# Kernel tuning notes

Measured on AMD Instinct MI355X. Metric: run time of the kernel, lower is better.

The kernel has to match this reference:

```python
import jax, jax.numpy as jnp
import numpy as np

BATCH, INPUT_SIZE, STEPS = 256, 512, 256
HIDDEN = 512


def setup_inputs() -> dict:
    key = jax.random.key(0)
    ks = jax.random.split(key, 5)
    s = 1.0 / np.sqrt(HIDDEN)
    return {
        "x": jax.random.normal(ks[0], (BATCH, INPUT_SIZE, STEPS), dtype=jnp.float32),
        "weight_ih": jax.random.uniform(ks[1], (3 * HIDDEN, INPUT_SIZE), jnp.float32, -s, s),
        "weight_hh": jax.random.uniform(ks[2], (3 * HIDDEN, HIDDEN), jnp.float32, -s, s),
        "bias_ih": jax.random.uniform(ks[3], (3 * HIDDEN,), jnp.float32, -s, s),
        "bias_hh": jax.random.uniform(ks[4], (3 * HIDDEN,), jnp.float32, -s, s),
    }


def reference(x, weight_ih, weight_hh, bias_ih, bias_hh):
    # x: [B, input_size, steps]; run a GRUCell over the time axis, return final hidden.
    B = x.shape[0]
    # Precompute all input projections in one big GEMM: [steps, B, 3H]
    gi_all = jnp.einsum('bis,gi->sbg', x, weight_ih) + bias_ih

    def step(h, gi):
        gh = h @ weight_hh.T + bias_hh  # [B, 3H]
        i_r, i_z, i_n = jnp.split(gi, 3, axis=-1)
        h_r, h_z, h_n = jnp.split(gh, 3, axis=-1)
        r = jax.nn.sigmoid(i_r + h_r)
        z = jax.nn.sigmoid(i_z + h_z)
        n = jnp.tanh(i_n + r * h_n)
        h_new = (1.0 - z) * n + z * h
        return h_new, None

    h0 = jnp.zeros((B, HIDDEN), dtype=x.dtype)
    h_final, _ = jax.lax.scan(step, h0, gi_all)
    return h_final
```

## Files before the change

### kernel.cpp

```cpp
#include <hip/hip_runtime.h>
#include <stdint.h>

typedef __attribute__((ext_vector_type(8))) short bf16x8;
typedef __attribute__((ext_vector_type(4))) short s16x4;
typedef __attribute__((ext_vector_type(4))) float f32x4;
typedef __attribute__((ext_vector_type(4))) unsigned u32x4;

#define AS1 __attribute__((address_space(1)))
#define AS3 __attribute__((address_space(3)))

static __device__ __forceinline__ void gload_lds16(const void* g, void* l) {
  __builtin_amdgcn_global_load_lds((const AS1 unsigned int*)g,
                                   (AS3 unsigned int*)l, 16, 0, 0);
}

static __device__ __forceinline__ short f2bs(float f) {
  unsigned u = __builtin_bit_cast(unsigned, f);
  unsigned r = (u + 0x7fffu + ((u >> 16) & 1u)) >> 16;
  return (short)r;
}
static __device__ __forceinline__ float bs2f(short s) {
  unsigned u = ((unsigned)(unsigned short)s) << 16;
  return __builtin_bit_cast(float, u);
}

static __device__ __forceinline__ float sigmoid_f(float x) {
  return 1.0f / (1.0f + __expf(-x));
}
static __device__ __forceinline__ float tanh_f(float x) {
  float ax = fabsf(x);
  float e  = __expf(-2.0f * ax);
  float t  = (1.0f - e) / (1.0f + e);
  return copysignf(t, x);
}

#define BATCH 256
#define HID   512
#define STEPS 256
#define G3    1536

__global__ __launch_bounds__(256) void convert_kernel(const float* __restrict__ src,
                                                      short* __restrict__ dst, int n4) {
  int i = blockIdx.x * 256 + threadIdx.x;
  if (i < n4) {
    float4 v = *(const float4*)(src + (size_t)i * 4);
    s16x4 o;
    o[0] = f2bs(v.x); o[1] = f2bs(v.y); o[2] = f2bs(v.z); o[3] = f2bs(v.w);
    *(s16x4*)(dst + (size_t)i * 4) = o;
  }
}

__global__ __launch_bounds__(256) void transpose_kernel(const float* __restrict__ x,
                                                        short* __restrict__ xT) {
  int bx = blockIdx.x;
  int st = bx & 7, it = (bx >> 3) & 15, b = bx >> 7;
  int s0 = st * 32, i0 = it * 32;
  int tid = threadIdx.x;
  __shared__ float tile[32][33];
  int il = tid >> 3, s4 = (tid & 7) * 4;
  float4 v = *(const float4*)(x + (size_t)b * 131072 + (size_t)(i0 + il) * 256 + s0 + s4);
  tile[il][s4 + 0] = v.x; tile[il][s4 + 1] = v.y;
  tile[il][s4 + 2] = v.z; tile[il][s4 + 3] = v.w;
  __syncthreads();
  int sl = tid >> 3, iv = (tid & 7) * 4;
  s16x4 o;
  o[0] = f2bs(tile[iv + 0][sl]); o[1] = f2bs(tile[iv + 1][sl]);
  o[2] = f2bs(tile[iv + 2][sl]); o[3] = f2bs(tile[iv + 3][sl]);
  *(s16x4*)(xT + (size_t)(s0 + sl) * 131072 + (size_t)b * 512 + i0 + iv) = o;
}

__global__ __launch_bounds__(256) void phase1_kernel(const short* __restrict__ A,
                                                     const short* __restrict__ B,
                                                     const float* __restrict__ bias,
                                                     short* __restrict__ out, int M) {
  int MT = M >> 7;
  int bx = blockIdx.x;
  int mt = bx % MT, nt = bx / MT;
  int m0 = mt * 128, n0 = nt * 128;
  int tid = threadIdx.x, w = tid >> 6, lane = tid & 63;
  int lm = lane & 15, q = lane >> 4;
  int wm = w & 1, wn = w >> 1;
  __shared__ short As[128 * 32];
  __shared__ short Bs[128 * 32];
  f32x4 acc[4][4] = {};
  int srow = lane >> 2;
  int scol = (lane & 3) * 8;

  for (int kt = 0; kt < 16; ++kt) {
#pragma unroll
    for (int i2 = 0; i2 < 2; ++i2) {
      int i = w * 2 + i2;
      int row = i * 16 + srow;
      gload_lds16(A + (size_t)(m0 + row) * 512 + kt * 32 + scol, As + i * 512);
      gload_lds16(B + (size_t)(n0 + row) * 512 + kt * 32 + scol, Bs + i * 512);
    }
    __syncthreads();
    bf16x8 av[4], bv[4];
#pragma unroll
    for (int f = 0; f < 4; ++f) {
      av[f] = *(const bf16x8*)(As + (wm * 64 + f * 16 + lm) * 32 + q * 8);
      bv[f] = *(const bf16x8*)(Bs + (wn * 64 + f * 16 + lm) * 32 + q * 8);
    }
#pragma unroll
    for (int fm = 0; fm < 4; ++fm)
#pragma unroll
      for (int fn = 0; fn < 4; ++fn)
        acc[fm][fn] = __builtin_amdgcn_mfma_f32_16x16x32_bf16(av[fm], bv[fn], acc[fm][fn], 0, 0, 0);
    __syncthreads();
  }
#pragma unroll
  for (int fn = 0; fn < 4; ++fn) {
    int g = n0 + wn * 64 + fn * 16 + lm;
    float bi = bias[g];
#pragma unroll
    for (int fm = 0; fm < 4; ++fm) {
      int rb = m0 + wm * 64 + fm * 16 + q * 4;
#pragma unroll
      for (int r = 0; r < 4; ++r)
        out[(size_t)(rb + r) * G3 + g] = f2bs(acc[fm][fn][r] + bi);
    }
  }
}

__global__ __launch_bounds__(256) void scan_kernel(const short* __restrict__ gi,
                                                   const short* __restrict__ Whh,
                                                   const float* __restrict__ bias_hh,
                                                   unsigned* __restrict__ hbuf,
                                                   float* __restrict__ hmaster,
                                                   int CH, int step_base, int first) {
  int bid = blockIdx.x;
  int xcd = bid & 7, slot = bid >> 3;
  int group = xcd + 8 * (slot >> 4);
  int j = slot & 15;
  int tid = threadIdx.x;
  int w = tid >> 6, lane = tid & 63;
  int lm = lane & 15, q = lane >> 4;
  int grow = group * 16;

  __shared__ short h_lds[16 * 520];
  __shared__ float gh_lds[16][100];
  __shared__ float h_loc[512];
  __shared__ float bhh[96];

  bf16x8 Bf[2][16];
  if (w < 3) {
#pragma unroll
    for (int tau = 0; tau < 2; ++tau)
#pragma unroll
      for (int kt = 0; kt < 16; ++kt) {
        int row = w * 512 + j * 32 + tau * 16 + lm;
        Bf[tau][kt] = *(const bf16x8*)(Whh + (size_t)row * 512 + kt * 32 + q * 8);
      }
  }

  if (tid < 96) {
    int p = tid >> 5, cc = tid & 31;
    bhh[tid] = bias_hh[p * 512 + j * 32 + cc];
  }
#pragma unroll
  for (int u = 0; u < 2; ++u) {
    int idx = tid + u * 256;
    int r = idx >> 5, cc = idx & 31;
    h_loc[idx] = first ? 0.0f : hmaster[(size_t)(grow + r) * 512 + j * 32 + cc];
  }
  __syncthreads();

  int i0 = tid, i1 = tid + 256;
  const short* gp0 = gi + (size_t)(grow + (i0 >> 5)) * G3 + j * 32 + (i0 & 31);
  const short* gp1 = gi + (size_t)(grow + (i1 >> 5)) * G3 + j * 32 + (i1 & 31);
  const size_t gstride = (size_t)256 * G3;

  short pg0r = gp0[0], pg0z = gp0[512], pg0n = gp0[1024];
  short pg1r = gp1[0], pg1z = gp1[512], pg1n = gp1[1024];

  unsigned o0 = (unsigned)tid * 16u;
  const int r0 = tid >> 7;
  const int colb = (tid & 127) * 4;
  short* lp = h_lds + r0 * 520 + colb;
  unsigned* grp_base = hbuf + (size_t)group * 8192;

  for (int t = 0; t < CH; ++t) {
    int gstep = step_base + t;
    int p = gstep & 1;
    const unsigned* src = grp_base + (size_t)p * 131072;
    unsigned want = (unsigned)gstep;

    u32x4 v0, v1, v2, v3, v4, v5, v6, v7;
    int spin = 0;
    for (;;) {
      asm volatile(
          "global_load_dwordx4 %0, %8, %16 sc0 sc1\n\t"
          "global_load_dwordx4 %1, %9, %16 sc0 sc1\n\t"
          "global_load_dwordx4 %2, %10, %16 sc0 sc1\n\t"
          "global_load_dwordx4 %3, %11, %16 sc0 sc1\n\t"
          "global_load_dwordx4 %4, %12, %16 sc0 sc1\n\t"
          "global_load_dwordx4 %5, %13, %16 sc0 sc1\n\t"
          "global_load_dwordx4 %6, %14, %16 sc0 sc1\n\t"
          "global_load_dwordx4 %7, %15, %16 sc0 sc1\n\t"
          "s_waitcnt vmcnt(0)"
          : "=&v"(v0), "=&v"(v1), "=&v"(v2), "=&v"(v3),
            "=&v"(v4), "=&v"(v5), "=&v"(v6), "=&v"(v7)
          : "v"(o0), "v"(o0 + 4096u), "v"(o0 + 8192u), "v"(o0 + 12288u),
            "v"(o0 + 16384u), "v"(o0 + 20480u), "v"(o0 + 24576u), "v"(o0 + 28672u),
            "s"(src)
          : "memory");
      unsigned d;
      d  = (v0[0] ^ want) | (v0[1] ^ want) | (v0[2] ^ want) | (v0[3] ^ want);
      d |= (v1[0] ^ want) | (v1[1] ^ want) | (v1[2] ^ want) | (v1[3] ^ want);
      d |= (v2[0] ^ want) | (v2[1] ^ want) | (v2[2] ^ want) | (v2[3] ^ want);
      d |= (v3[0] ^ want) | (v3[1] ^ want) | (v3[2] ^ want) | (v3[3] ^ want);
      d |= (v4[0] ^ want) | (v4[1] ^ want) | (v4[2] ^ want) | (v4[3] ^ want);
      d |= (v5[0] ^ want) | (v5[1] ^ want) | (v5[2] ^ want) | (v5[3] ^ want);
      d |= (v6[0] ^ want) | (v6[1] ^ want) | (v6[2] ^ want) | (v6[3] ^ want);
      d |= (v7[0] ^ want) | (v7[1] ^ want) | (v7[2] ^ want) | (v7[3] ^ want);
      if (((d & 0xffffu) == 0u) || (++spin > (1 << 16))) break;
      __builtin_amdgcn_s_sleep(1);
    }

#define STASH(vv, c)                                                         \
    {                                                                        \
      s16x4 o_;                                                              \
      o_[0] = (short)(vv[0] >> 16); o_[1] = (short)(vv[1] >> 16);            \
      o_[2] = (short)(vv[2] >> 16); o_[3] = (short)(vv[3] >> 16);            \
      *(s16x4*)(lp + (c) * 1040) = o_;                                       \
    }
    STASH(v0, 0) STASH(v1, 1) STASH(v2, 2) STASH(v3, 3)
    STASH(v4, 4) STASH(v5, 5) STASH(v6, 6) STASH(v7, 7)
#undef STASH

    float cg0r = bs2f(pg0r), cg0z = bs2f(pg0z), cg0n = bs2f(pg0n);
    float cg1r = bs2f(pg1r), cg1z = bs2f(pg1z), cg1n = bs2f(pg1n);
    {
      size_t o = (size_t)((t + 1 < CH) ? (t + 1) : t) * gstride;
      pg0r = gp0[o]; pg0z = gp0[o + 512]; pg0n = gp0[o + 1024];
      pg1r = gp1[o]; pg1z = gp1[o + 512]; pg1n = gp1[o + 1024];
    }
    __syncthreads();

    if (w < 3) {
      f32x4 a0 = {0.f,0.f,0.f,0.f}, a1 = {0.f,0.f,0.f,0.f};
      f32x4 a2 = {0.f,0.f,0.f,0.f}, a3 = {0.f,0.f,0.f,0.f};
#pragma unroll
      for (int kt = 0; kt < 8; ++kt) {
        bf16x8 a = *(const bf16x8*)(h_lds + lm * 520 + kt * 32 + q * 8);
        a0 = __builtin_amdgcn_mfma_f32_16x16x32_bf16(a, Bf[0][kt], a0, 0, 0, 0);
        a1 = __builtin_amdgcn_mfma_f32_16x16x32_bf16(a, Bf[1][kt], a1, 0, 0, 0);
      }
#pragma unroll
      for (int kt = 8; kt < 16; ++kt) {
        bf16x8 a = *(const bf16x8*)(h_lds + lm * 520 + kt * 32 + q * 8);
        a2 = __builtin_amdgcn_mfma_f32_16x16x32_bf16(a, Bf[0][kt], a2, 0, 0, 0);
        a3 = __builtin_amdgcn_mfma_f32_16x16x32_bf16(a, Bf[1][kt], a3, 0, 0, 0);
      }
#pragma unroll
      for (int r = 0; r < 4; ++r) {
        gh_lds[q * 4 + r][w * 32 + lm]      = a0[r] + a2[r];
        gh_lds[q * 4 + r][w * 32 + 16 + lm] = a1[r] + a3[r];
      }
    }
    __syncthreads();

    unsigned tagp = (unsigned)(gstep + 1);
    unsigned* dstb = grp_base + (size_t)(1 - p) * 131072;
    {
      int r = i0 >> 5, cc = i0 & 31;
      float hr = gh_lds[r][cc]      + bhh[cc];
      float hz = gh_lds[r][32 + cc] + bhh[32 + cc];
      float hn = gh_lds[r][64 + cc] + bhh[64 + cc];
      float rr = sigmoid_f(cg0r + hr);
      float zz = sigmoid_f(cg0z + hz);
      float nn = tanh_f(cg0n + rr * hn);
      float hv = (1.0f - zz) * nn + zz * h_loc[i0];
      h_loc[i0] = hv;
      unsigned val = (((unsigned)(unsigned short)f2bs(hv)) << 16) | tagp;
      unsigned* dp = dstb + r * 512 + j * 32 + cc;
      asm volatile("global_store_dword %0, %1, off sc0 sc1" :: "v"(dp), "v"(val) : "memory");
    }
    {
      int r = i1 >> 5, cc = i1 & 31;
      float hr = gh_lds[r][cc]      + bhh[cc];
      float hz = gh_lds[r][32 + cc] + bhh[32 + cc];
      float hn = gh_lds[r][64 + cc] + bhh[64 + cc];
      float rr = sigmoid_f(cg1r + hr);
      float zz = sigmoid_f(cg1z + hz);
      float nn = tanh_f(cg1n + rr * hn);
      float hv = (1.0f - zz) * nn + zz * h_loc[i1];
      h_loc[i1] = hv;
      unsigned val = (((unsigned)(unsigned short)f2bs(hv)) << 16) | tagp;
      unsigned* dp = dstb + r * 512 + j * 32 + cc;
      asm volatile("global_store_dword %0, %1, off sc0 sc1" :: "v"(dp), "v"(val) : "memory");
    }
  }

#pragma unroll
  for (int u = 0; u < 2; ++u) {
    int idx = tid + u * 256;
    int r = idx >> 5, cc = idx & 31;
    hmaster[(size_t)(grow + r) * 512 + j * 32 + cc] = h_loc[idx];
  }
}

extern "C" void kernel_launch(void* const* d_in, const int* in_sizes, int n_in,
                              void* d_out, int out_size, void* d_ws, size_t ws_size,
                              hipStream_t stream) {
  const float* x   = (const float*)d_in[0];
  const float* Wih = (const float*)d_in[1];
  const float* Whh = (const float*)d_in[2];
  const float* bih = (const float*)d_in[3];
  const float* bhh = (const float*)d_in[4];
  float* out = (float*)d_out;
  char* ws = (char*)d_ws;

  const size_t XT_BYTES   = (size_t)256 * 256 * 512 * 2;
  const size_t W_BYTES    = (size_t)1536 * 512 * 2;
  const size_t HBUF_BYTES = (size_t)2 * 256 * 512 * 4;
  const size_t FIXED = XT_BYTES + 2 * W_BYTES + HBUF_BYTES + 4096;

  int CH = 256;
  while (CH > 4 && FIXED + (size_t)CH * 256 * G3 * 2 > ws_size) CH >>= 1;

  size_t off = 0;
  short* gi = (short*)(ws + off);          off += (size_t)CH * 256 * G3 * 2;
  short* xT = (short*)(ws + off);          off += XT_BYTES;
  short* WihB = (short*)(ws + off);        off += W_BYTES;
  short* WhhB = (short*)(ws + off);        off += W_BYTES;
  unsigned* hbuf = (unsigned*)(ws + off);

  hipMemsetAsync(hbuf, 0, HBUF_BYTES, stream);

  convert_kernel<<<768, 256, 0, stream>>>(Wih, WihB, 196608);
  convert_kernel<<<768, 256, 0, stream>>>(Whh, WhhB, 196608);
  transpose_kernel<<<32768, 256, 0, stream>>>(x, xT);

  int nch = 256 / CH;
  for (int c = 0; c < nch; ++c) {
    int M = CH * 256;
    phase1_kernel<<<(M / 128) * 12, 256, 0, stream>>>(
        xT + (size_t)c * CH * 256 * 512, WihB, bih, gi, M);
    scan_kernel<<<256, 256, 0, stream>>>(gi, WhhB, bhh, hbuf, out,
                                         CH, c * CH, c == 0 ? 1 : 0);
  }
}
```

Measured before the change: 888.6 us.

## Split recurrent GEMM over K across all four waves, feed MFMA directly from registers

Each of the four waves now holds a K-quarter of the W_hh slice for all six output tiles and builds MFMA A-operands straight from the polled hidden-state registers, skipping the LDS staging of h. Partial sums are written to a double-buffered LDS area and reduced in the gate epilogue, which removes one __syncthreads per step and puts the fourth, previously idle wave to work. The cost is an extra cross-wave reduction over LDS and a changed polling address pattern. The spin limit is also halved.

```diff
diff --git a/kernel.cpp b/kernel.cpp
--- a/kernel.cpp
+++ b/kernel.cpp
@@ -32,6 +32,11 @@
   float e  = __expf(-2.0f * ax);
   float t  = (1.0f - e) / (1.0f + e);
   return copysignf(t, x);
+}
+
+static __device__ __forceinline__ unsigned stale8(u32x4 a, u32x4 b, unsigned want) {
+  return ((a[0] ^ want) | (a[1] ^ want) | (a[2] ^ want) | (a[3] ^ want) |
+          (b[0] ^ want) | (b[1] ^ want) | (b[2] ^ want) | (b[3] ^ want)) & 0xffffu;
 }
 
 #define BATCH 256
@@ -129,34 +134,28 @@
                                                    float* __restrict__ hmaster,
                                                    int CH, int step_base, int first) {
   int bid = blockIdx.x;
-  int xcd = bid & 7, slot = bid >> 3;
-  int group = xcd + 8 * (slot >> 4);
-  int j = slot & 15;
+  int group = (bid & 7) + 8 * ((bid >> 3) >> 4);
+  int j = (bid >> 3) & 15;
   int tid = threadIdx.x;
   int w = tid >> 6, lane = tid & 63;
   int lm = lane & 15, q = lane >> 4;
   int grow = group * 16;
 
-  __shared__ short h_lds[16 * 520];
-  __shared__ float gh_lds[16][100];
+  __shared__ float part[12288];
   __shared__ float h_loc[512];
   __shared__ float bhh[96];
 
-  bf16x8 Bf[2][16];
-  if (w < 3) {
-#pragma unroll
-    for (int tau = 0; tau < 2; ++tau)
-#pragma unroll
-      for (int kt = 0; kt < 16; ++kt) {
-        int row = w * 512 + j * 32 + tau * 16 + lm;
-        Bf[tau][kt] = *(const bf16x8*)(Whh + (size_t)row * 512 + kt * 32 + q * 8);
-      }
-  }
-
-  if (tid < 96) {
-    int p = tid >> 5, cc = tid & 31;
-    bhh[tid] = bias_hh[p * 512 + j * 32 + cc];
-  }
+  bf16x8 Wf[6][4];
+#pragma unroll
+  for (int n = 0; n < 6; ++n) {
+    int g = n >> 1, ch = n & 1;
+#pragma unroll
+    for (int i = 0; i < 4; ++i) {
+      int k = w * 4 + i;
+      Wf[n][i] = *(const bf16x8*)(Whh + (size_t)(g * 512 + j * 32 + ch * 16 + lm) * 512 + k * 32 + q * 8);
+    }
+  }
+  if (tid < 96) bhh[tid] = bias_hh[(tid >> 5) * 512 + j * 32 + (tid & 31)];
 #pragma unroll
   for (int u = 0; u < 2; ++u) {
     int idx = tid + u * 256;
@@ -169,64 +168,61 @@
   const short* gp0 = gi + (size_t)(grow + (i0 >> 5)) * G3 + j * 32 + (i0 & 31);
   const short* gp1 = gi + (size_t)(grow + (i1 >> 5)) * G3 + j * 32 + (i1 & 31);
   const size_t gstride = (size_t)256 * G3;
-
   short pg0r = gp0[0], pg0z = gp0[512], pg0n = gp0[1024];
   short pg1r = gp1[0], pg1z = gp1[512], pg1n = gp1[1024];
 
-  unsigned o0 = (unsigned)tid * 16u;
-  const int r0 = tid >> 7;
-  const int colb = (tid & 127) * 4;
-  short* lp = h_lds + r0 * 520 + colb;
-  unsigned* grp_base = hbuf + (size_t)group * 8192;
+  unsigned* grp = hbuf + (size_t)group * 8192;
+  unsigned o0 = (unsigned)(lm * 2048 + w * 512 + q * 32);
+  unsigned o1 = o0 + 128, o2 = o0 + 256, o3 = o0 + 384;
 
   for (int t = 0; t < CH; ++t) {
     int gstep = step_base + t;
     int p = gstep & 1;
-    const unsigned* src = grp_base + (size_t)p * 131072;
-    unsigned want = (unsigned)gstep;
+    const unsigned* src = grp + (size_t)p * 131072;
+    unsigned want = (unsigned)gstep & 0xffffu;
 
     u32x4 v0, v1, v2, v3, v4, v5, v6, v7;
     int spin = 0;
     for (;;) {
       asm volatile(
-          "global_load_dwordx4 %0, %8, %16 sc0 sc1\n\t"
-          "global_load_dwordx4 %1, %9, %16 sc0 sc1\n\t"
-          "global_load_dwordx4 %2, %10, %16 sc0 sc1\n\t"
-          "global_load_dwordx4 %3, %11, %16 sc0 sc1\n\t"
-          "global_load_dwordx4 %4, %12, %16 sc0 sc1\n\t"
-          "global_load_dwordx4 %5, %13, %16 sc0 sc1\n\t"
-          "global_load_dwordx4 %6, %14, %16 sc0 sc1\n\t"
-          "global_load_dwordx4 %7, %15, %16 sc0 sc1\n\t"
+          "global_load_dwordx4 %0, %8, %12 sc0 sc1\n\t"
+          "global_load_dwordx4 %1, %8, %12 offset:16 sc0 sc1\n\t"
+          "global_load_dwordx4 %2, %9, %12 sc0 sc1\n\t"
+          "global_load_dwordx4 %3, %9, %12 offset:16 sc0 sc1\n\t"
+          "global_load_dwordx4 %4, %10, %12 sc0 sc1\n\t"
+          "global_load_dwordx4 %5, %10, %12 offset:16 sc0 sc1\n\t"
+          "global_load_dwordx4 %6, %11, %12 sc0 sc1\n\t"
+          "global_load_dwordx4 %7, %11, %12 offset:16 sc0 sc1\n\t"
           "s_waitcnt vmcnt(0)"
           : "=&v"(v0), "=&v"(v1), "=&v"(v2), "=&v"(v3),
             "=&v"(v4), "=&v"(v5), "=&v"(v6), "=&v"(v7)
-          : "v"(o0), "v"(o0 + 4096u), "v"(o0 + 8192u), "v"(o0 + 12288u),
-            "v"(o0 + 16384u), "v"(o0 + 20480u), "v"(o0 + 24576u), "v"(o0 + 28672u),
-            "s"(src)
+          : "v"(o0), "v"(o1), "v"(o2), "v"(o3), "s"(src)
           : "memory");
-      unsigned d;
-      d  = (v0[0] ^ want) | (v0[1] ^ want) | (v0[2] ^ want) | (v0[3] ^ want);
-      d |= (v1[0] ^ want) | (v1[1] ^ want) | (v1[2] ^ want) | (v1[3] ^ want);
-      d |= (v2[0] ^ want) | (v2[1] ^ want) | (v2[2] ^ want) | (v2[3] ^ want);
-      d |= (v3[0] ^ want) | (v3[1] ^ want) | (v3[2] ^ want) | (v3[3] ^ want);
-      d |= (v4[0] ^ want) | (v4[1] ^ want) | (v4[2] ^ want) | (v4[3] ^ want);
-      d |= (v5[0] ^ want) | (v5[1] ^ want) | (v5[2] ^ want) | (v5[3] ^ want);
-      d |= (v6[0] ^ want) | (v6[1] ^ want) | (v6[2] ^ want) | (v6[3] ^ want);
-      d |= (v7[0] ^ want) | (v7[1] ^ want) | (v7[2] ^ want) | (v7[3] ^ want);
-      if (((d & 0xffffu) == 0u) || (++spin > (1 << 16))) break;
+      unsigned d = stale8(v0, v1, want) | stale8(v2, v3, want) |
+                   stale8(v4, v5, want) | stale8(v6, v7, want);
+      if (d == 0u || ++spin > (1 << 15)) break;
       __builtin_amdgcn_s_sleep(1);
     }
 
-#define STASH(vv, c)                                                         \
-    {                                                                        \
-      s16x4 o_;                                                              \
-      o_[0] = (short)(vv[0] >> 16); o_[1] = (short)(vv[1] >> 16);            \
-      o_[2] = (short)(vv[2] >> 16); o_[3] = (short)(vv[3] >> 16);            \
-      *(s16x4*)(lp + (c) * 1040) = o_;                                       \
-    }
-    STASH(v0, 0) STASH(v1, 1) STASH(v2, 2) STASH(v3, 3)
-    STASH(v4, 4) STASH(v5, 5) STASH(v6, 6) STASH(v7, 7)
-#undef STASH
+    f32x4 acc[6] = {};
+
+#define SLICE(ii, VA, VB)                                                     \
+    {                                                                         \
+      bf16x8 a;                                                               \
+      a[0] = (short)(VA[0] >> 16); a[1] = (short)(VA[1] >> 16);               \
+      a[2] = (short)(VA[2] >> 16); a[3] = (short)(VA[3] >> 16);               \
+      a[4] = (short)(VB[0] >> 16); a[5] = (short)(VB[1] >> 16);               \
+      a[6] = (short)(VB[2] >> 16); a[7] = (short)(VB[3] >> 16);               \
+      _Pragma("unroll")                                                       \
+      for (int n = 0; n < 6; ++n)                                             \
+        acc[n] = __builtin_amdgcn_mfma_f32_16x16x32_bf16(a, Wf[n][ii], acc[n], 0, 0, 0); \
+    }
+
+    SLICE(0, v0, v1)
+    SLICE(1, v2, v3)
+    SLICE(2, v4, v5)
+    SLICE(3, v6, v7)
+#undef SLICE
 
     float cg0r = bs2f(pg0r), cg0z = bs2f(pg0z), cg0n = bs2f(pg0n);
     float cg1r = bs2f(pg1r), cg1z = bs2f(pg1z), cg1n = bs2f(pg1n);
@@ -235,61 +231,44 @@
       pg0r = gp0[o]; pg0z = gp0[o + 512]; pg0n = gp0[o + 1024];
       pg1r = gp1[o]; pg1z = gp1[o + 512]; pg1n = gp1[o + 1024];
     }
+
+    {
+      float* pw = part + p * 6144 + w * 1536 + lane * 4;
+#pragma unroll
+      for (int n = 0; n < 6; ++n)
+        *(f32x4*)(pw + n * 256) = acc[n];
+    }
     __syncthreads();
 
-    if (w < 3) {
-      f32x4 a0 = {0.f,0.f,0.f,0.f}, a1 = {0.f,0.f,0.f,0.f};
-      f32x4 a2 = {0.f,0.f,0.f,0.f}, a3 = {0.f,0.f,0.f,0.f};
-#pragma unroll
-      for (int kt = 0; kt < 8; ++kt) {
-        bf16x8 a = *(const bf16x8*)(h_lds + lm * 520 + kt * 32 + q * 8);
-        a0 = __builtin_amdgcn_mfma_f32_16x16x32_bf16(a, Bf[0][kt], a0, 0, 0, 0);
-        a1 = __builtin_amdgcn_mfma_f32_16x16x32_bf16(a, Bf[1][kt], a1, 0, 0, 0);
-      }
-#pragma unroll
-      for (int kt = 8; kt < 16; ++kt) {
-        bf16x8 a = *(const bf16x8*)(h_lds + lm * 520 + kt * 32 + q * 8);
-        a2 = __builtin_amdgcn_mfma_f32_16x16x32_bf16(a, Bf[0][kt], a2, 0, 0, 0);
-        a3 = __builtin_amdgcn_mfma_f32_16x16x32_bf16(a, Bf[1][kt], a3, 0, 0, 0);
-      }
-#pragma unroll
-      for (int r = 0; r < 4; ++r) {
-        gh_lds[q * 4 + r][w * 32 + lm]      = a0[r] + a2[r];
-        gh_lds[q * 4 + r][w * 32 + 16 + lm] = a1[r] + a3[r];
-      }
-    }
-    __syncthreads();
-
     unsigned tagp = (unsigned)(gstep + 1);
-    unsigned* dstb = grp_base + (size_t)(1 - p) * 131072;
-    {
-      int r = i0 >> 5, cc = i0 & 31;
-      float hr = gh_lds[r][cc]      + bhh[cc];
-      float hz = gh_lds[r][32 + cc] + bhh[32 + cc];
-      float hn = gh_lds[r][64 + cc] + bhh[64 + cc];
-      float rr = sigmoid_f(cg0r + hr);
-      float zz = sigmoid_f(cg0z + hz);
-      float nn = tanh_f(cg0n + rr * hn);
-      float hv = (1.0f - zz) * nn + zz * h_loc[i0];
-      h_loc[i0] = hv;
-      unsigned val = (((unsigned)(unsigned short)f2bs(hv)) << 16) | tagp;
-      unsigned* dp = dstb + r * 512 + j * 32 + cc;
-      asm volatile("global_store_dword %0, %1, off sc0 sc1" :: "v"(dp), "v"(val) : "memory");
-    }
-    {
-      int r = i1 >> 5, cc = i1 & 31;
-      float hr = gh_lds[r][cc]      + bhh[cc];
-      float hz = gh_lds[r][32 + cc] + bhh[32 + cc];
-      float hn = gh_lds[r][64 + cc] + bhh[64 + cc];
-      float rr = sigmoid_f(cg1r + hr);
-      float zz = sigmoid_f(cg1z + hz);
-      float nn = tanh_f(cg1n + rr * hn);
-      float hv = (1.0f - zz) * nn + zz * h_loc[i1];
-      h_loc[i1] = hv;
-      unsigned val = (((unsigned)(unsigned short)f2bs(hv)) << 16) | tagp;
-      unsigned* dp = dstb + r * 512 + j * 32 + cc;
-      asm volatile("global_store_dword %0, %1, off sc0 sc1" :: "v"(dp), "v"(val) : "memory");
-    }
+    unsigned* dstb = grp + (size_t)(1 - p) * 131072;
+
+#define CELL(EE, CGR, CGZ, CGN)                                               \
+    {                                                                         \
+      int row = (EE) >> 5, colh = (EE) & 31;                                  \
+      const float* pp = part + p * 6144 + ((row >> 2) * 16 + (colh & 15)) * 4 \
+                        + (row & 3);                                          \
+      int nr = colh >> 4;                                                     \
+      float sr = 0.f, sz = 0.f, sn = 0.f;                                     \
+      _Pragma("unroll")                                                       \
+      for (int ww = 0; ww < 4; ++ww) {                                        \
+        const float* qq = pp + ww * 1536;                                     \
+        sr += qq[nr * 256]; sz += qq[(2 + nr) * 256]; sn += qq[(4 + nr) * 256]; \
+      }                                                                       \
+      float hr = sr + bhh[colh], hz = sz + bhh[32 + colh], hn = sn + bhh[64 + colh]; \
+      float rr = sigmoid_f(CGR + hr);                                         \
+      float zz = sigmoid_f(CGZ + hz);                                         \
+      float nn = tanh_f(CGN + rr * hn);                                       \
+      float hv = (1.0f - zz) * nn + zz * h_loc[EE];                           \
+      h_loc[EE] = hv;                                                         \
+      unsigned val = (((unsigned)(unsigned short)f2bs(hv)) << 16) | tagp;     \
+      unsigned* dp = dstb + row * 512 + j * 32 + colh;                        \
+      asm volatile("global_store_dword %0, %1, off sc0 sc1" :: "v"(dp), "v"(val) : "memory"); \
+    }
+
+    CELL(i0, cg0r, cg0z, cg0n)
+    CELL(i1, cg1r, cg1z, cg1n)
+#undef CELL
   }
 
 #pragma unroll
```

Result: slower. 1.173 ms (+32.0%).

## Repartition GRU scan into fewer, wider blocks with all waves doing MFMA

Applied to the files above, without the earlier changes.

The recurrent scan kernel goes from 256 blocks of 256 threads, each owning 32 hidden columns with 3 MFMA waves, to 64 blocks of 512 threads. Each block owns 128 hidden columns for a 16-row batch group, and all 8 waves compute all three gates over the full K of 512. This cuts the number of blocks that poll and publish hidden state each step and gives each block a larger share of the work. The cost is more weight registers per wave (48 fragments), a longer serial K chain per wave, and fewer CUs in use, which may reduce parallelism per step. The poll loop also loads half as much data per thread and has a lower spin cap.

```diff
diff --git a/kernel.cpp b/kernel.cpp
--- a/kernel.cpp
+++ b/kernel.cpp
@@ -32,6 +32,11 @@
   float e  = __expf(-2.0f * ax);
   float t  = (1.0f - e) / (1.0f + e);
   return copysignf(t, x);
+}
+
+static __device__ __forceinline__ unsigned stale8(u32x4 a, u32x4 b, unsigned want) {
+  return ((a[0] ^ want) | (a[1] ^ want) | (a[2] ^ want) | (a[3] ^ want) |
+          (b[0] ^ want) | (b[1] ^ want) | (b[2] ^ want) | (b[3] ^ want)) & 0xffffu;
 }
 
 #define BATCH 256
@@ -122,98 +127,78 @@
   }
 }
 
-__global__ __launch_bounds__(256) void scan_kernel(const short* __restrict__ gi,
-                                                   const short* __restrict__ Whh,
-                                                   const float* __restrict__ bias_hh,
-                                                   unsigned* __restrict__ hbuf,
-                                                   float* __restrict__ hmaster,
-                                                   int CH, int step_base, int first) {
+__global__ __launch_bounds__(512, 2) void scan_kernel(const short* __restrict__ gi,
+                                                      const short* __restrict__ Whh,
+                                                      const float* __restrict__ bias_hh,
+                                                      unsigned* __restrict__ hbuf,
+                                                      float* __restrict__ hmaster,
+                                                      int CH, int step_base, int first) {
   int bid = blockIdx.x;
   int xcd = bid & 7, slot = bid >> 3;
-  int group = xcd + 8 * (slot >> 4);
-  int j = slot & 15;
+  int j = slot & 3;
+  int group = xcd + 8 * (slot >> 2);
   int tid = threadIdx.x;
   int w = tid >> 6, lane = tid & 63;
   int lm = lane & 15, q = lane >> 4;
   int grow = group * 16;
 
   __shared__ short h_lds[16 * 520];
-  __shared__ float gh_lds[16][100];
-  __shared__ float h_loc[512];
-  __shared__ float bhh[96];
-
-  bf16x8 Bf[2][16];
-  if (w < 3) {
-#pragma unroll
-    for (int tau = 0; tau < 2; ++tau)
-#pragma unroll
-      for (int kt = 0; kt < 16; ++kt) {
-        int row = w * 512 + j * 32 + tau * 16 + lm;
-        Bf[tau][kt] = *(const bf16x8*)(Whh + (size_t)row * 512 + kt * 32 + q * 8);
-      }
-  }
-
-  if (tid < 96) {
-    int p = tid >> 5, cc = tid & 31;
-    bhh[tid] = bias_hh[p * 512 + j * 32 + cc];
-  }
-#pragma unroll
-  for (int u = 0; u < 2; ++u) {
-    int idx = tid + u * 256;
-    int r = idx >> 5, cc = idx & 31;
-    h_loc[idx] = first ? 0.0f : hmaster[(size_t)(grow + r) * 512 + j * 32 + cc];
+  __shared__ float gh_lds[16][388];
+  __shared__ float h_loc[2048];
+  __shared__ float bhh[384];
+
+  bf16x8 Wf[3][16];
+#pragma unroll
+  for (int g = 0; g < 3; ++g)
+#pragma unroll
+    for (int kt = 0; kt < 16; ++kt)
+      Wf[g][kt] = *(const bf16x8*)(Whh + (size_t)(g * 512 + j * 128 + w * 16 + lm) * 512 + kt * 32 + q * 8);
+
+  if (tid < 384) bhh[tid] = bias_hh[(tid >> 7) * 512 + j * 128 + (tid & 127)];
+#pragma unroll
+  for (int u = 0; u < 4; ++u) {
+    int idx = tid + u * 512;
+    int r = idx >> 7, cc = idx & 127;
+    h_loc[idx] = first ? 0.0f : hmaster[(size_t)(grow + r) * 512 + j * 128 + cc];
   }
   __syncthreads();
 
-  int i0 = tid, i1 = tid + 256;
-  const short* gp0 = gi + (size_t)(grow + (i0 >> 5)) * G3 + j * 32 + (i0 & 31);
-  const short* gp1 = gi + (size_t)(grow + (i1 >> 5)) * G3 + j * 32 + (i1 & 31);
+  const short* gp[4];
+#pragma unroll
+  for (int u = 0; u < 4; ++u) {
+    int idx = tid + u * 512;
+    gp[u] = gi + (size_t)(grow + (idx >> 7)) * G3 + j * 128 + (idx & 127);
+  }
   const size_t gstride = (size_t)256 * G3;
-
-  short pg0r = gp0[0], pg0z = gp0[512], pg0n = gp0[1024];
-  short pg1r = gp1[0], pg1z = gp1[512], pg1n = gp1[1024];
-
+  short pgr[4], pgz[4], pgn[4];
+#pragma unroll
+  for (int u = 0; u < 4; ++u) { pgr[u] = gp[u][0]; pgz[u] = gp[u][512]; pgn[u] = gp[u][1024]; }
+
+  unsigned* grp = hbuf + (size_t)group * 8192;
   unsigned o0 = (unsigned)tid * 16u;
-  const int r0 = tid >> 7;
-  const int colb = (tid & 127) * 4;
-  short* lp = h_lds + r0 * 520 + colb;
-  unsigned* grp_base = hbuf + (size_t)group * 8192;
+  short* lp = h_lds + (tid >> 7) * 520 + (tid & 127) * 4;
 
   for (int t = 0; t < CH; ++t) {
     int gstep = step_base + t;
     int p = gstep & 1;
-    const unsigned* src = grp_base + (size_t)p * 131072;
-    unsigned want = (unsigned)gstep;
-
-    u32x4 v0, v1, v2, v3, v4, v5, v6, v7;
+    const unsigned* src = grp + (size_t)p * 131072;
+    unsigned want = (unsigned)gstep & 0xffffu;
+
+    u32x4 v0, v1, v2, v3;
     int spin = 0;
     for (;;) {
       asm volatile(
-          "global_load_dwordx4 %0, %8, %16 sc0 sc1\n\t"
-          "global_load_dwordx4 %1, %9, %16 sc0 sc1\n\t"
-          "global_load_dwordx4 %2, %10, %16 sc0 sc1\n\t"
-          "global_load_dwordx4 %3, %11, %16 sc0 sc1\n\t"
-          "global_load_dwordx4 %4, %12, %16 sc0 sc1\n\t"
-          "global_load_dwordx4 %5, %13, %16 sc0 sc1\n\t"
-          "global_load_dwordx4 %6, %14, %16 sc0 sc1\n\t"
-          "global_load_dwordx4 %7, %15, %16 sc0 sc1\n\t"
+          "global_load_dwordx4 %0, %4, %8 sc0 sc1\n\t"
+          "global_load_dwordx4 %1, %5, %8 sc0 sc1\n\t"
+          "global_load_dwordx4 %2, %6, %8 sc0 sc1\n\t"
+          "global_load_dwordx4 %3, %7, %8 sc0 sc1\n\t"
           "s_waitcnt vmcnt(0)"
-          : "=&v"(v0), "=&v"(v1), "=&v"(v2), "=&v"(v3),
-            "=&v"(v4), "=&v"(v5), "=&v"(v6), "=&v"(v7)
-          : "v"(o0), "v"(o0 + 4096u), "v"(o0 + 8192u), "v"(o0 + 12288u),
-            "v"(o0 + 16384u), "v"(o0 + 20480u), "v"(o0 + 24576u), "v"(o0 + 28672u),
+          : "=&v"(v0), "=&v"(v1), "=&v"(v2), "=&v"(v3)
+          : "v"(o0), "v"(o0 + 8192u), "v"(o0 + 16384u), "v"(o0 + 24576u),
             "s"(src)
           : "memory");
-      unsigned d;
-      d  = (v0[0] ^ want) | (v0[1] ^ want) | (v0[2] ^ want) | (v0[3] ^ want);
-      d |= (v1[0] ^ want) | (v1[1] ^ want) | (v1[2] ^ want) | (v1[3] ^ want);
-      d |= (v2[0] ^ want) | (v2[1] ^ want) | (v2[2] ^ want) | (v2[3] ^ want);
-      d |= (v3[0] ^ want) | (v3[1] ^ want) | (v3[2] ^ want) | (v3[3] ^ want);
-      d |= (v4[0] ^ want) | (v4[1] ^ want) | (v4[2] ^ want) | (v4[3] ^ want);
-      d |= (v5[0] ^ want) | (v5[1] ^ want) | (v5[2] ^ want) | (v5[3] ^ want);
-      d |= (v6[0] ^ want) | (v6[1] ^ want) | (v6[2] ^ want) | (v6[3] ^ want);
-      d |= (v7[0] ^ want) | (v7[1] ^ want) | (v7[2] ^ want) | (v7[3] ^ want);
-      if (((d & 0xffffu) == 0u) || (++spin > (1 << 16))) break;
+      unsigned d = stale8(v0, v1, want) | stale8(v2, v3, want);
+      if (d == 0u || ++spin > (1 << 15)) break;
       __builtin_amdgcn_s_sleep(1);
     }
 
@@ -222,81 +207,66 @@
       s16x4 o_;                                                              \
       o_[0] = (short)(vv[0] >> 16); o_[1] = (short)(vv[1] >> 16);            \
       o_[2] = (short)(vv[2] >> 16); o_[3] = (short)(vv[3] >> 16);            \
-      *(s16x4*)(lp + (c) * 1040) = o_;                                       \
+      *(s16x4*)(lp + (c) * 2080) = o_;                                       \
     }
     STASH(v0, 0) STASH(v1, 1) STASH(v2, 2) STASH(v3, 3)
-    STASH(v4, 4) STASH(v5, 5) STASH(v6, 6) STASH(v7, 7)
 #undef STASH
 
-    float cg0r = bs2f(pg0r), cg0z = bs2f(pg0z), cg0n = bs2f(pg0n);
-    float cg1r = bs2f(pg1r), cg1z = bs2f(pg1z), cg1n = bs2f(pg1n);
+    float cgr[4], cgz[4], cgn[4];
+#pragma unroll
+    for (int u = 0; u < 4; ++u) { cgr[u] = bs2f(pgr[u]); cgz[u] = bs2f(pgz[u]); cgn[u] = bs2f(pgn[u]); }
     {
       size_t o = (size_t)((t + 1 < CH) ? (t + 1) : t) * gstride;
-      pg0r = gp0[o]; pg0z = gp0[o + 512]; pg0n = gp0[o + 1024];
-      pg1r = gp1[o]; pg1z = gp1[o + 512]; pg1n = gp1[o + 1024];
+#pragma unroll
+      for (int u = 0; u < 4; ++u) {
+        pgr[u] = gp[u][o]; pgz[u] = gp[u][o + 512]; pgn[u] = gp[u][o + 1024];
+      }
     }
     __syncthreads();
 
-    if (w < 3) {
-      f32x4 a0 = {0.f,0.f,0.f,0.f}, a1 = {0.f,0.f,0.f,0.f};
-      f32x4 a2 = {0.f,0.f,0.f,0.f}, a3 = {0.f,0.f,0.f,0.f};
-#pragma unroll
-      for (int kt = 0; kt < 8; ++kt) {
+    {
+      f32x4 a0 = {0.f,0.f,0.f,0.f}, a1 = {0.f,0.f,0.f,0.f}, a2 = {0.f,0.f,0.f,0.f};
+#pragma unroll
+      for (int kt = 0; kt < 16; ++kt) {
         bf16x8 a = *(const bf16x8*)(h_lds + lm * 520 + kt * 32 + q * 8);
-        a0 = __builtin_amdgcn_mfma_f32_16x16x32_bf16(a, Bf[0][kt], a0, 0, 0, 0);
-        a1 = __builtin_amdgcn_mfma_f32_16x16x32_bf16(a, Bf[1][kt], a1, 0, 0, 0);
+        a0 = __builtin_amdgcn_mfma_f32_16x16x32_bf16(a, Wf[0][kt], a0, 0, 0, 0);
+        a1 = __builtin_amdgcn_mfma_f32_16x16x32_bf16(a, Wf[1][kt], a1, 0, 0, 0);
+        a2 = __builtin_amdgcn_mfma_f32_16x16x32_bf16(a, Wf[2][kt], a2, 0, 0, 0);
       }
 #pragma unroll
-      for (int kt = 8; kt < 16; ++kt) {
-        bf16x8 a = *(const bf16x8*)(h_lds + lm * 520 + kt * 32 + q * 8);
-        a2 = __builtin_amdgcn_mfma_f32_16x16x32_bf16(a, Bf[0][kt], a2, 0, 0, 0);
-        a3 = __builtin_amdgcn_mfma_f32_16x16x32_bf16(a, Bf[1][kt], a3, 0, 0, 0);
+      for (int r = 0; r < 4; ++r) {
+        gh_lds[q * 4 + r][w * 16 + lm]       = a0[r];
+        gh_lds[q * 4 + r][128 + w * 16 + lm] = a1[r];
+        gh_lds[q * 4 + r][256 + w * 16 + lm] = a2[r];
       }
-#pragma unroll
-      for (int r = 0; r < 4; ++r) {
-        gh_lds[q * 4 + r][w * 32 + lm]      = a0[r] + a2[r];
-        gh_lds[q * 4 + r][w * 32 + 16 + lm] = a1[r] + a3[r];
-      }
     }
     __syncthreads();
 
     unsigned tagp = (unsigned)(gstep + 1);
-    unsigned* dstb = grp_base + (size_t)(1 - p) * 131072;
-    {
-      int r = i0 >> 5, cc = i0 & 31;
-      float hr = gh_lds[r][cc]      + bhh[cc];
-      float hz = gh_lds[r][32 + cc] + bhh[32 + cc];
-      float hn = gh_lds[r][64 + cc] + bhh[64 + cc];
-      float rr = sigmoid_f(cg0r + hr);
-      float zz = sigmoid_f(cg0z + hz);
-      float nn = tanh_f(cg0n + rr * hn);
-      float hv = (1.0f - zz) * nn + zz * h_loc[i0];
-      h_loc[i0] = hv;
+    unsigned* dstb = grp + (size_t)(1 - p) * 131072;
+#pragma unroll
+    for (int u = 0; u < 4; ++u) {
+      int idx = tid + u * 512;
+      int row = idx >> 7, col = idx & 127;
+      float hr = gh_lds[row][col]       + bhh[col];
+      float hz = gh_lds[row][128 + col] + bhh[128 + col];
+      float hn = gh_lds[row][256 + col] + bhh[256 + col];
+      float rr = sigmoid_f(cgr[u] + hr);
+      float zz = sigmoid_f(cgz[u] + hz);
+      float nn = tanh_f(cgn[u] + rr * hn);
+      float hv = (1.0f - zz) * nn + zz * h_loc[idx];
+      h_loc[idx] = hv;
       unsigned val = (((unsigned)(unsigned short)f2bs(hv)) << 16) | tagp;
-      unsigned* dp = dstb + r * 512 + j * 32 + cc;
+      unsigned* dp = dstb + row * 512 + j * 128 + col;
       asm volatile("global_store_dword %0, %1, off sc0 sc1" :: "v"(dp), "v"(val) : "memory");
     }
-    {
-      int r = i1 >> 5, cc = i1 & 31;
-      float hr = gh_lds[r][cc]      + bhh[cc];
-      float hz = gh_lds[r][32 + cc] + bhh[32 + cc];
-      float hn = gh_lds[r][64 + cc] + bhh[64 + cc];
-      float rr = sigmoid_f(cg1r + hr);
-      float zz = sigmoid_f(cg1z + hz);
-      float nn = tanh_f(cg1n + rr * hn);
-      float hv = (1.0f - zz) * nn + zz * h_loc[i1];
-      h_loc[i1] = hv;
-      unsigned val = (((unsigned)(unsigned short)f2bs(hv)) << 16) | tagp;
-      unsigned* dp = dstb + r * 512 + j * 32 + cc;
-      asm volatile("global_store_dword %0, %1, off sc0 sc1" :: "v"(dp), "v"(val) : "memory");
-    }
-  }
-
-#pragma unroll
-  for (int u = 0; u < 2; ++u) {
-    int idx = tid + u * 256;
-    int r = idx >> 5, cc = idx & 31;
-    hmaster[(size_t)(grow + r) * 512 + j * 32 + cc] = h_loc[idx];
+  }
+
+#pragma unroll
+  for (int u = 0; u < 4; ++u) {
+    int idx = tid + u * 512;
+    int r = idx >> 7, cc = idx & 127;
+    hmaster[(size_t)(grow + r) * 512 + j * 128 + cc] = h_loc[idx];
   }
 }
 
@@ -337,7 +307,7 @@
     int M = CH * 256;
     phase1_kernel<<<(M / 128) * 12, 256, 0, stream>>>(
         xT + (size_t)c * CH * 256 * 512, WihB, bih, gi, M);
-    scan_kernel<<<256, 256, 0, stream>>>(gi, WhhB, bhh, hbuf, out,
-                                         CH, c * CH, c == 0 ? 1 : 0);
-  }
-}
+    scan_kernel<<<64, 512, 0, stream>>>(gi, WhhB, bhh, hbuf, out,
+                                        CH, c * CH, c == 0 ? 1 : 0);
+  }
+}
```

New measurement: 1.439 ms. 61.9% more time.
